# Optimization experiments

Hardware: AMD Instinct MI355X
Metric: run time of the kernel (lower is better)

The kernel has to match this reference:

```python
import jax, jax.numpy as jnp
import numpy as np


def setup_inputs() -> dict:
    key = jax.random.key(0)
    ks = jax.random.split(key, 8)
    B, Q, K, F, FV, C = 8, 2048, 2048, 512, 512, 2
    q = jax.random.normal(ks[0], (B, Q, F), dtype=jnp.float32)
    k = jax.random.normal(ks[1], (B, K, F), dtype=jnp.float32)
    v = jax.random.normal(ks[2], (B, K, FV), dtype=jnp.float32)
    coords_q = jax.random.uniform(ks[3], (B, Q, C), dtype=jnp.float32)
    coords_k = jax.random.uniform(ks[4], (B, K, C), dtype=jnp.float32)
    attn_mask = jax.random.randint(ks[5], (B, Q, K), 0, 2).astype(bool)
    alibi_mask = jax.random.randint(ks[6], (B, Q, K), 0, 2).astype(bool)
    bias_scale = jax.random.uniform(ks[7], (1,), dtype=jnp.float32)
    return {"q": q, "k": k, "v": v, "coords_q": coords_q, "coords_k": coords_k,
            "attn_mask": attn_mask, "alibi_mask": alibi_mask, "bias_scale": bias_scale}


def reference(q, k, v, coords_q, coords_k, attn_mask, alibi_mask, bias_scale):
    # scaled dot-product logits: [B, Q, K]
    scale = k.shape[-1] ** -0.5
    weight_logits = jnp.einsum('bqf,bkf->bqk', q, k) * scale
    # pairwise Euclidean coordinate distances: [B, Q, K]
    diff = coords_q[:, :, None, :] - coords_k[:, None, :, :]
    distances = jnp.linalg.norm(diff, axis=-1)
    # _RunningMeanScaler in eval mode divides by running_mean == 1 (identity)
    scaled_distances = distances * bias_scale  # bias_scale broadcasts from [1]
    scaled_distances = jnp.where(alibi_mask, 0.0, scaled_distances)
    weights = jax.nn.softmax(weight_logits, axis=-1)
    # post-softmax bias subtraction + masking (non-standard attention)
    weights = jnp.where(attn_mask, 0.0, weights - scaled_distances)
    attention = jnp.einsum('bqk,bkf->bqf', weights, v)
    return attention
```

## Files before the change

kernel.cpp:

```cpp
#include <hip/hip_runtime.h>
#include <hip/hip_bf16.h>
#include <math.h>

#define BN  8
#define QN  2048
#define KN  2048
#define FN  512
#define FVN 512

typedef __bf16 bf16x8 __attribute__((ext_vector_type(8)));
typedef __bf16 bf16x4v __attribute__((ext_vector_type(4)));
typedef float  f32x4  __attribute__((ext_vector_type(4)));

__device__ inline bf16x8 pack8(float4 a, float4 b) {
  bf16x8 r;
  r[0] = (__bf16)a.x; r[1] = (__bf16)a.y; r[2] = (__bf16)a.z; r[3] = (__bf16)a.w;
  r[4] = (__bf16)b.x; r[5] = (__bf16)b.y; r[6] = (__bf16)b.z; r[7] = (__bf16)b.w;
  return r;
}

__device__ __forceinline__ void g2l16(const __bf16* g, __bf16* l) {
  __builtin_amdgcn_global_load_lds(
      (const __attribute__((address_space(1))) void*)g,
      (__attribute__((address_space(3))) void*)l,
      16, 0, 0);
}

__global__ __launch_bounds__(256) void prep(
    const float* __restrict__ qm, const float* __restrict__ km,
    const float* __restrict__ vm,
    __bf16* __restrict__ qb, __bf16* __restrict__ kb, __bf16* __restrict__ Vt) {
  const int tid = threadIdx.x;
  if (blockIdx.y == 0) {
    const size_t idx = ((size_t)blockIdx.x * 256 + tid) * 8;
    const float scale = 0.044194173824159216f;
    float4 a = *(const float4*)(qm + idx);
    float4 b = *(const float4*)(qm + idx + 4);
    a.x *= scale; a.y *= scale; a.z *= scale; a.w *= scale;
    b.x *= scale; b.y *= scale; b.z *= scale; b.w *= scale;
    *(bf16x8*)(qb + idx) = pack8(a, b);
  } else if (blockIdx.y == 1) {
    const size_t idx = ((size_t)blockIdx.x * 256 + tid) * 8;
    float4 a = *(const float4*)(km + idx);
    float4 b = *(const float4*)(km + idx + 4);
    *(bf16x8*)(kb + idx) = pack8(a, b);
  } else {
    const int bx = blockIdx.x;
    if (bx >= (KN / 64) * (FVN / 64) * BN) return;
    const int b  = bx >> 8;
    const int f0 = ((bx >> 5) & 7) * 64;
    const int k0 = (bx & 31) * 64;
    __shared__ float tile[64][65];
    const int r = tid >> 4;
    const int c = (tid & 15) * 4;
#pragma unroll
    for (int i = 0; i < 4; i++) {
      float4 u = *(const float4*)(vm + ((size_t)b * KN + k0 + r + i * 16) * FVN + f0 + c);
      tile[r + i * 16][c] = u.x; tile[r + i * 16][c + 1] = u.y;
      tile[r + i * 16][c + 2] = u.z; tile[r + i * 16][c + 3] = u.w;
    }
    __syncthreads();
#pragma unroll
    for (int i = 0; i < 4; i++) {
      int fv = r + i * 16;
      bf16x4v w;
      w[0] = (__bf16)tile[c][fv];     w[1] = (__bf16)tile[c + 1][fv];
      w[2] = (__bf16)tile[c + 2][fv]; w[3] = (__bf16)tile[c + 3][fv];
      *(bf16x4v*)(Vt + ((size_t)b * FVN + f0 + fv) * KN + k0 + c) = w;
    }
  }
}

__global__ __launch_bounds__(256) void gemm_s(
    const __bf16* __restrict__ qb, const __bf16* __restrict__ kb,
    __bf16* __restrict__ Sws, float* __restrict__ sums,
    int b0, int q0, int qchunk) {
  __shared__ __align__(16) __bf16 As[2][128][32];
  __shared__ __align__(16) __bf16 Bs[2][128][32];
  const int tid = threadIdx.x;
  const int lane = tid & 63, wave = tid >> 6;
  const int wq = (wave & 1) * 64, wk = (wave >> 1) * 64;
  const int qt = blockIdx.x * 128, kt = blockIdx.y * 128;
  const int z = blockIdx.z, b = b0 + z;
  __bf16* S = Sws + (size_t)z * qchunk * KN;
  const __bf16* Ab = qb + ((size_t)b * QN + q0 + qt) * FN;
  const __bf16* Bb = kb + ((size_t)b * KN + kt) * FN;
  const int srow = lane >> 2;
  const int scol = (lane & 3) * 8;
  const int r = lane & 15, quad = lane >> 4;
  f32x4 acc[4][4] = {};
  for (int f0 = 0; f0 < FN; f0 += 64) {
    __syncthreads();
#pragma unroll
    for (int h = 0; h < 2; h++) {
      const int co = f0 + h * 32 + scol;
      g2l16(Ab + (size_t)(wave * 32 + srow) * FN + co,      &As[h][wave * 32][0]);
      g2l16(Ab + (size_t)(wave * 32 + 16 + srow) * FN + co, &As[h][wave * 32 + 16][0]);
      g2l16(Bb + (size_t)(wave * 32 + srow) * FN + co,      &Bs[h][wave * 32][0]);
      g2l16(Bb + (size_t)(wave * 32 + 16 + srow) * FN + co, &Bs[h][wave * 32 + 16][0]);
    }
    __syncthreads();
#pragma unroll
    for (int h = 0; h < 2; h++) {
      bf16x8 af[4], bf[4];
#pragma unroll
      for (int i = 0; i < 4; i++) af[i] = *(bf16x8*)&As[h][wq + i * 16 + r][quad * 8];
#pragma unroll
      for (int j = 0; j < 4; j++) bf[j] = *(bf16x8*)&Bs[h][wk + j * 16 + r][quad * 8];
#pragma unroll
      for (int i = 0; i < 4; i++)
#pragma unroll
        for (int j = 0; j < 4; j++)
          acc[i][j] = __builtin_amdgcn_mfma_f32_16x16x32_bf16(af[i], bf[j], acc[i][j], 0, 0, 0);
    }
  }
#pragma unroll
  for (int i = 0; i < 4; i++)
#pragma unroll
    for (int t = 0; t < 4; t++) {
      float e = 0.f;
#pragma unroll
      for (int j = 0; j < 4; j++) {
        __bf16 sb = (__bf16)acc[i][j][t];
        S[(size_t)(qt + wq + i * 16 + quad * 4 + t) * KN + (kt + wk + j * 16 + r)] = sb;
        e += __expf((float)sb);
      }
      e += __shfl_xor(e, 1); e += __shfl_xor(e, 2);
      e += __shfl_xor(e, 4); e += __shfl_xor(e, 8);
      if (r == 0)
        atomicAdd(&sums[(size_t)z * qchunk + qt + wq + i * 16 + quad * 4 + t], e);
    }
}

__global__ __launch_bounds__(256) void gemm_wv(
    const __bf16* __restrict__ S, const float* __restrict__ sums,
    const __bf16* __restrict__ Vt,
    const float* __restrict__ cq, const float* __restrict__ ck,
    const int* __restrict__ attn, const int* __restrict__ alibi,
    const float* __restrict__ bsp, float* __restrict__ out,
    int b0, int q0, int qchunk) {
  __shared__ __align__(16) __bf16 Ws[64][32];
  __shared__ __align__(16) __bf16 Vs[512][32];
  const int tid = threadIdx.x;
  const int lane = tid & 63, wave = tid >> 6;
  const int qt = blockIdx.x * 64;
  const int z = blockIdx.z, b = b0 + z;
  const int wr = tid >> 2;
  const int wc = (tid & 3) * 8;
  const int qg = q0 + qt + wr;
  const float qx = cq[((size_t)b * QN + qg) * 2 + 0];
  const float qy = cq[((size_t)b * QN + qg) * 2 + 1];
  const float inv = 1.0f / sums[(size_t)z * qchunk + qt + wr];
  const float bs = bsp[0];
  const __bf16* Srow = S + ((size_t)z * qchunk + qt + wr) * KN;
  const int* arow = attn + ((size_t)b * QN + qg) * KN;
  const int* lrow = alibi + ((size_t)b * QN + qg) * KN;
  const float* ckb = ck + (size_t)b * KN * 2;
  const __bf16* Vb = Vt + ((size_t)b * FVN + wave * 128) * KN;
  const int srow = lane >> 2, scol = (lane & 3) * 8;
  const int r = lane & 15, quad = lane >> 4;
  f32x4 acc[4][8] = {};
  for (int k0 = 0; k0 < KN; k0 += 32) {
    bf16x8 s8 = *(const bf16x8*)(Srow + k0 + wc);
    int4 am0 = *(const int4*)(arow + k0 + wc);
    int4 am1 = *(const int4*)(arow + k0 + wc + 4);
    int4 al0 = *(const int4*)(lrow + k0 + wc);
    int4 al1 = *(const int4*)(lrow + k0 + wc + 4);
    float4 c0 = *(const float4*)(ckb + (size_t)(k0 + wc) * 2);
    float4 c1 = *(const float4*)(ckb + (size_t)(k0 + wc) * 2 + 4);
    float4 c2 = *(const float4*)(ckb + (size_t)(k0 + wc) * 2 + 8);
    float4 c3 = *(const float4*)(ckb + (size_t)(k0 + wc) * 2 + 12);
    int   am[8] = {am0.x, am0.y, am0.z, am0.w, am1.x, am1.y, am1.z, am1.w};
    int   al[8] = {al0.x, al0.y, al0.z, al0.w, al1.x, al1.y, al1.z, al1.w};
    float kx[8] = {c0.x, c0.z, c1.x, c1.z, c2.x, c2.z, c3.x, c3.z};
    float ky[8] = {c0.y, c0.w, c1.y, c1.w, c2.y, c2.w, c3.y, c3.w};
    bf16x8 w8;
#pragma unroll
    for (int j = 0; j < 8; j++) {
      float dx = qx - kx[j], dy = qy - ky[j];
      float sd = al[j] ? 0.f : sqrtf(dx * dx + dy * dy) * bs;
      float w = am[j] ? 0.f : (__expf((float)s8[j]) * inv - sd);
      w8[j] = (__bf16)w;
    }
    __syncthreads();
    *(bf16x8*)&Ws[wr][wc] = w8;
#pragma unroll
    for (int h = 0; h < 8; h++)
      g2l16(Vb + (size_t)(h * 16 + srow) * KN + k0 + scol, &Vs[wave * 128 + h * 16][0]);
    __syncthreads();
    bf16x8 af[4];
#pragma unroll
    for (int i = 0; i < 4; i++) af[i] = *(bf16x8*)&Ws[i * 16 + r][quad * 8];
#pragma unroll
    for (int j = 0; j < 8; j++) {
      bf16x8 bfv = *(bf16x8*)&Vs[wave * 128 + j * 16 + r][quad * 8];
#pragma unroll
      for (int i = 0; i < 4; i++)
        acc[i][j] = __builtin_amdgcn_mfma_f32_16x16x32_bf16(af[i], bfv, acc[i][j], 0, 0, 0);
    }
  }
#pragma unroll
  for (int i = 0; i < 4; i++)
#pragma unroll
    for (int j = 0; j < 8; j++)
#pragma unroll
      for (int t = 0; t < 4; t++) {
        int qq = q0 + qt + i * 16 + quad * 4 + t;
        int fv = wave * 128 + j * 16 + r;
        out[((size_t)b * QN + qq) * FVN + fv] = acc[i][j][t];
      }
}

extern "C" void kernel_launch(void* const* d_in, const int* in_sizes, int n_in,
                              void* d_out, int out_size, void* d_ws, size_t ws_size,
                              hipStream_t stream) {
  (void)in_sizes; (void)n_in; (void)out_size;
  const float* qm   = (const float*)d_in[0];
  const float* km   = (const float*)d_in[1];
  const float* vm   = (const float*)d_in[2];
  const float* cq   = (const float*)d_in[3];
  const float* ck   = (const float*)d_in[4];
  const int*   attn = (const int*)d_in[5];
  const int*   alibi= (const int*)d_in[6];
  const float* bsp  = (const float*)d_in[7];
  float* out = (float*)d_out;

  __bf16* qb  = (__bf16*)d_ws;
  __bf16* kb  = qb + (size_t)BN * QN * FN;
  __bf16* Vt  = kb + (size_t)BN * KN * FN;
  const size_t fixed = ((size_t)BN * QN * FN + (size_t)BN * KN * FN +
                        (size_t)BN * FVN * KN) * 2;
  int nb = BN, qc = QN;
  while (nb > 1 && fixed + (size_t)nb * qc * (KN * 2 + 4) > ws_size) nb >>= 1;
  while (qc > 128 && fixed + (size_t)nb * qc * (KN * 2 + 4) > ws_size) qc >>= 1;
  __bf16* Sws  = Vt + (size_t)BN * FVN * KN;
  float*  sums = (float*)((char*)Sws + (size_t)nb * qc * KN * 2);

  prep<<<dim3((BN * QN * FN) / 2048, 3), 256, 0, stream>>>(qm, km, vm, qb, kb, Vt);
  for (int b0 = 0; b0 < BN; b0 += nb) {
    for (int q0 = 0; q0 < QN; q0 += qc) {
      hipMemsetAsync(sums, 0, (size_t)nb * qc * 4, stream);
      gemm_s<<<dim3(qc / 128, KN / 128, nb), 256, 0, stream>>>(qb, kb, Sws, sums, b0, q0, qc);
      gemm_wv<<<dim3(qc / 64, 1, nb), 256, 0, stream>>>(Sws, sums, Vt, cq, ck,
                                                        attn, alibi, bsp, out, b0, q0, qc);
    }
  }
}
```

Before: 535.5 us.

## Retile gemm_wv to 32-row tiles with 512 threads for more blocks

```diff
diff --git a/kernel.cpp b/kernel.cpp
--- a/kernel.cpp
+++ b/kernel.cpp
@@ -10,6 +10,7 @@
 
 typedef __bf16 bf16x8 __attribute__((ext_vector_type(8)));
 typedef __bf16 bf16x4v __attribute__((ext_vector_type(4)));
+typedef __bf16 bf16x2v __attribute__((ext_vector_type(2)));
 typedef float  f32x4  __attribute__((ext_vector_type(4)));
 
 __device__ inline bf16x8 pack8(float4 a, float4 b) {
@@ -132,21 +133,21 @@
     }
 }
 
-__global__ __launch_bounds__(256) void gemm_wv(
+__global__ __launch_bounds__(512) void gemm_wv(
     const __bf16* __restrict__ S, const float* __restrict__ sums,
     const __bf16* __restrict__ Vt,
     const float* __restrict__ cq, const float* __restrict__ ck,
     const int* __restrict__ attn, const int* __restrict__ alibi,
     const float* __restrict__ bsp, float* __restrict__ out,
     int b0, int q0, int qchunk) {
-  __shared__ __align__(16) __bf16 Ws[64][32];
+  __shared__ __align__(16) __bf16 Ws[32][32];
   __shared__ __align__(16) __bf16 Vs[512][32];
   const int tid = threadIdx.x;
   const int lane = tid & 63, wave = tid >> 6;
-  const int qt = blockIdx.x * 64;
+  const int qt = blockIdx.x * 32;
   const int z = blockIdx.z, b = b0 + z;
-  const int wr = tid >> 2;
-  const int wc = (tid & 3) * 8;
+  const int wr = tid >> 4;
+  const int wc = (tid & 15) * 2;
   const int qg = q0 + qt + wr;
   const float qx = cq[((size_t)b * QN + qg) * 2 + 0];
   const float qy = cq[((size_t)b * QN + qg) * 2 + 1];
@@ -156,57 +157,51 @@
   const int* arow = attn + ((size_t)b * QN + qg) * KN;
   const int* lrow = alibi + ((size_t)b * QN + qg) * KN;
   const float* ckb = ck + (size_t)b * KN * 2;
-  const __bf16* Vb = Vt + ((size_t)b * FVN + wave * 128) * KN;
+  const __bf16* Vb = Vt + (size_t)b * FVN * KN;
   const int srow = lane >> 2, scol = (lane & 3) * 8;
   const int r = lane & 15, quad = lane >> 4;
-  f32x4 acc[4][8] = {};
+  f32x4 acc[2][4] = {};
   for (int k0 = 0; k0 < KN; k0 += 32) {
-    bf16x8 s8 = *(const bf16x8*)(Srow + k0 + wc);
-    int4 am0 = *(const int4*)(arow + k0 + wc);
-    int4 am1 = *(const int4*)(arow + k0 + wc + 4);
-    int4 al0 = *(const int4*)(lrow + k0 + wc);
-    int4 al1 = *(const int4*)(lrow + k0 + wc + 4);
-    float4 c0 = *(const float4*)(ckb + (size_t)(k0 + wc) * 2);
-    float4 c1 = *(const float4*)(ckb + (size_t)(k0 + wc) * 2 + 4);
-    float4 c2 = *(const float4*)(ckb + (size_t)(k0 + wc) * 2 + 8);
-    float4 c3 = *(const float4*)(ckb + (size_t)(k0 + wc) * 2 + 12);
-    int   am[8] = {am0.x, am0.y, am0.z, am0.w, am1.x, am1.y, am1.z, am1.w};
-    int   al[8] = {al0.x, al0.y, al0.z, al0.w, al1.x, al1.y, al1.z, al1.w};
-    float kx[8] = {c0.x, c0.z, c1.x, c1.z, c2.x, c2.z, c3.x, c3.z};
-    float ky[8] = {c0.y, c0.w, c1.y, c1.w, c2.y, c2.w, c3.y, c3.w};
-    bf16x8 w8;
-#pragma unroll
-    for (int j = 0; j < 8; j++) {
-      float dx = qx - kx[j], dy = qy - ky[j];
-      float sd = al[j] ? 0.f : sqrtf(dx * dx + dy * dy) * bs;
-      float w = am[j] ? 0.f : (__expf((float)s8[j]) * inv - sd);
-      w8[j] = (__bf16)w;
-    }
-    __syncthreads();
-    *(bf16x8*)&Ws[wr][wc] = w8;
-#pragma unroll
-    for (int h = 0; h < 8; h++)
-      g2l16(Vb + (size_t)(h * 16 + srow) * KN + k0 + scol, &Vs[wave * 128 + h * 16][0]);
-    __syncthreads();
-    bf16x8 af[4];
-#pragma unroll
-    for (int i = 0; i < 4; i++) af[i] = *(bf16x8*)&Ws[i * 16 + r][quad * 8];
-#pragma unroll
-    for (int j = 0; j < 8; j++) {
-      bf16x8 bfv = *(bf16x8*)&Vs[wave * 128 + j * 16 + r][quad * 8];
-#pragma unroll
-      for (int i = 0; i < 4; i++)
+    bf16x2v s2 = *(const bf16x2v*)(Srow + k0 + wc);
+    int2 am2 = *(const int2*)(arow + k0 + wc);
+    int2 al2 = *(const int2*)(lrow + k0 + wc);
+    float4 cc = *(const float4*)(ckb + (size_t)(k0 + wc) * 2);
+    float w0, w1;
+    {
+      float dx = qx - cc.x, dy = qy - cc.y;
+      float sd = al2.x ? 0.f : sqrtf(dx * dx + dy * dy) * bs;
+      w0 = am2.x ? 0.f : (__expf((float)s2[0]) * inv - sd);
+      dx = qx - cc.z; dy = qy - cc.w;
+      sd = al2.y ? 0.f : sqrtf(dx * dx + dy * dy) * bs;
+      w1 = am2.y ? 0.f : (__expf((float)s2[1]) * inv - sd);
+    }
+    bf16x2v w2; w2[0] = (__bf16)w0; w2[1] = (__bf16)w1;
+    __syncthreads();
+    *(bf16x2v*)&Ws[wr][wc] = w2;
+#pragma unroll
+    for (int h = 0; h < 4; h++)
+      g2l16(Vb + (size_t)(wave * 64 + h * 16 + srow) * KN + k0 + scol,
+            &Vs[wave * 64 + h * 16][0]);
+    __syncthreads();
+    bf16x8 af[2];
+#pragma unroll
+    for (int i = 0; i < 2; i++) af[i] = *(bf16x8*)&Ws[i * 16 + r][quad * 8];
+#pragma unroll
+    for (int j = 0; j < 4; j++) {
+      bf16x8 bfv = *(bf16x8*)&Vs[wave * 64 + j * 16 + r][quad * 8];
+#pragma unroll
+      for (int i = 0; i < 2; i++)
         acc[i][j] = __builtin_amdgcn_mfma_f32_16x16x32_bf16(af[i], bfv, acc[i][j], 0, 0, 0);
     }
   }
 #pragma unroll
-  for (int i = 0; i < 4; i++)
-#pragma unroll
-    for (int j = 0; j < 8; j++)
+  for (int i = 0; i < 2; i++)
+#pragma unroll
+    for (int j = 0; j < 4; j++)
 #pragma unroll
       for (int t = 0; t < 4; t++) {
         int qq = q0 + qt + i * 16 + quad * 4 + t;
-        int fv = wave * 128 + j * 16 + r;
+        int fv = wave * 64 + j * 16 + r;
         out[((size_t)b * QN + qq) * FVN + fv] = acc[i][j][t];
       }
 }
@@ -241,7 +236,7 @@
     for (int q0 = 0; q0 < QN; q0 += qc) {
       hipMemsetAsync(sums, 0, (size_t)nb * qc * 4, stream);
       gemm_s<<<dim3(qc / 128, KN / 128, nb), 256, 0, stream>>>(qb, kb, Sws, sums, b0, q0, qc);
-      gemm_wv<<<dim3(qc / 64, 1, nb), 256, 0, stream>>>(Sws, sums, Vt, cq, ck,
+      gemm_wv<<<dim3(qc / 32, 1, nb), 512, 0, stream>>>(Sws, sums, Vt, cq, ck,
                                                         attn, alibi, bsp, out, b0, q0, qc);
     }
   }
```

New measurement: 514.5 us. -3.9%, faster.
